# Optimization experiments

Measured on AMD Instinct MI355X. Metric: run time of the kernel, lower is better.

The kernel has to match this reference:

```python
import jax, jax.numpy as jnp
from jax import lax
import numpy as np

B, K = 32, 8
NUM_LABELS = 600
GRID = 100          # grid_size
FEATURE_DIM = 256
HUMAN = 100         # human_width == human_height


def setup_inputs() -> dict:
    rng = np.random.default_rng(0)
    ids = rng.integers(0, NUM_LABELS, size=(B, K))
    # Synthetic OA_distn: per-label MVN params (means + Cholesky factors of small covs).
    # Means chosen so sampled obj_x/obj_y are non-negative (well-defined slicing regime).
    mean_xy = rng.uniform(0.2, 0.8, size=(NUM_LABELS, 2)).astype(np.float32)
    mean_wh = rng.uniform(-0.3, 0.3, size=(NUM_LABELS, 2)).astype(np.float32)
    L = 0.05 * np.eye(2, dtype=np.float32)  # shared Cholesky factor (cov = L L^T)
    eps_xy = rng.standard_normal((B, K, 2)).astype(np.float32)
    eps_wh = rng.standard_normal((B, K, 2)).astype(np.float32)
    d_xy = mean_xy[ids] + eps_xy @ L.T      # MVN sample per (b,k): mean + L eps
    d_wh = mean_wh[ids] + eps_wh @ L.T
    delta_x, delta_y = d_xy[..., 0], d_xy[..., 1]
    delta_w, delta_h = d_wh[..., 0], d_wh[..., 1]
    # .int() truncation as in torch
    obj_x = np.clip((delta_x * HUMAN).astype(np.int32), 0, None)
    obj_y = np.clip((delta_y * HUMAN).astype(np.int32), 0, None)
    obj_w = (HUMAN * np.exp(delta_w)).astype(np.int32)
    obj_h = (HUMAN * np.exp(delta_h)).astype(np.int32)
    # global canvas size: host-side max, mirrors .max().item()
    g_w = int(np.maximum(HUMAN, obj_x + obj_w).max())
    g_h = int(np.maximum(HUMAN, obj_y + obj_h).max())
    # learned params
    ks = jax.random.split(jax.random.key(0), 3)
    conv1_w = jax.random.normal(ks[0], (16, 2, 3, 3), jnp.float32) * 0.1
    conv1_b = jnp.zeros((16,), jnp.float32)
    conv2_w = jax.random.normal(ks[1], (32, 16, 3, 3), jnp.float32) * 0.05
    conv2_b = jnp.zeros((32,), jnp.float32)
    proj_w = jax.random.normal(ks[2], (FEATURE_DIM, 32 * GRID * GRID), jnp.float32) * 0.002
    proj_b = jnp.zeros((FEATURE_DIM,), jnp.float32)
    return {
        'obj_x': jnp.asarray(obj_x), 'obj_y': jnp.asarray(obj_y),
        'obj_w': jnp.asarray(obj_w), 'obj_h': jnp.asarray(obj_h),
        'g_h': g_h, 'g_w': g_w,
        'conv1_w': conv1_w, 'conv1_b': conv1_b,
        'conv2_w': conv2_w, 'conv2_b': conv2_b,
        'proj_w': proj_w, 'proj_b': proj_b,
    }


def _binary_maps(obj_x, obj_y, obj_w, obj_h, g_h, g_w):
    # Vectorized rectangle rasterization on the (g_h, g_w) global canvas.
    b, k = obj_x.shape
    yy = jnp.arange(g_h)[None, None, :, None]   # (1,1,gH,1)
    xx = jnp.arange(g_w)[None, None, None, :]   # (1,1,1,gW)
    human = jnp.broadcast_to(((yy < HUMAN) & (xx < HUMAN)), (b, k, g_h, g_w)).astype(jnp.float32)
    ox = obj_x[..., None, None]; oy = obj_y[..., None, None]
    ow = obj_w[..., None, None]; oh = obj_h[..., None, None]
    obj = ((yy >= oy) & (yy < oy + oh) & (xx >= ox) & (xx < ox + ow)).astype(jnp.float32)
    maps = jnp.stack((human, obj), axis=2).reshape(b * k, 2, g_h, g_w)
    # bilinear, half-pixel centers, no antialias == torch F.interpolate(align_corners=False)
    return jax.image.resize(maps, (b * k, 2, GRID, GRID), method='bilinear', antialias=False)


def reference(obj_x, obj_y, obj_w, obj_h, g_h, g_w, conv1_w, conv1_b, conv2_w, conv2_b, proj_w, proj_b):
    b, k = obj_x.shape
    maps = _binary_maps(obj_x, obj_y, obj_w, obj_h, g_h, g_w)  # (B*K,2,GRID,GRID)
    dn = ('NCHW', 'OIHW', 'NCHW')
    x = lax.conv_general_dilated(maps, conv1_w, (1, 1), 'SAME', dimension_numbers=dn) + conv1_b[None, :, None, None]
    x = lax.conv_general_dilated(x, conv2_w, (1, 1), 'SAME', dimension_numbers=dn) + conv2_b[None, :, None, None]
    x = x.reshape(b * k, -1)                     # (B*K, 32*GRID*GRID), CHW order
    out = x @ proj_w.T + proj_b                  # (B*K, FEATURE_DIM)
    return out.reshape(b, k, FEATURE_DIM)
```

## Files before the change

kernel.cpp:

```cpp
#include <hip/hip_runtime.h>
#include <cstddef>

#define NS 256
#define NF 256
#define NC1 16
#define NC2 32

__global__ __launch_bounds__(256) void k_prep(
    const int* __restrict__ obx, const int* __restrict__ oby,
    const int* __restrict__ obw, const int* __restrict__ obh,
    const int* __restrict__ ghp, const int* __restrict__ gwp,
    const float* __restrict__ w1, const float* __restrict__ w2,
    const float* __restrict__ pb,
    float* __restrict__ pyT, float* __restrict__ pxT,
    float* __restrict__ hy, float* __restrict__ hx,
    float* __restrict__ Weff, float* __restrict__ base) {
  int tid = threadIdx.x;
  if (blockIdx.x == 0) {
    int n = tid;
    float gh = (float)ghp[0], gw = (float)gwp[0];
    float sy = gh / 100.0f, sx = gw / 100.0f;
    int x0 = obx[n], y0 = oby[n], w = obw[n], h = obh[n];
    for (int j = 0; j < 100; ++j) {
      float u = (j + 0.5f) * sx - 0.5f;
      int a0 = (int)floorf(u);
      float t = u - (float)a0;
      float v0 = (a0 >= x0 && a0 < x0 + w) ? 1.f : 0.f;
      float v1 = (a0 + 1 >= x0 && a0 + 1 < x0 + w) ? 1.f : 0.f;
      pxT[j * 256 + n] = (1.f - t) * v0 + t * v1;
      u = (j + 0.5f) * sy - 0.5f;
      a0 = (int)floorf(u);
      t = u - (float)a0;
      v0 = (a0 >= y0 && a0 < y0 + h) ? 1.f : 0.f;
      v1 = (a0 + 1 >= y0 && a0 + 1 < y0 + h) ? 1.f : 0.f;
      pyT[j * 256 + n] = (1.f - t) * v0 + t * v1;
    }
    if (n < 100) {
      int j = n;
      float u = (j + 0.5f) * sx - 0.5f;
      int a0 = (int)floorf(u);
      float t = u - (float)a0;
      float v0 = (a0 >= 0 && a0 < 100) ? 1.f : 0.f;
      float v1 = (a0 + 1 >= 0 && a0 + 1 < 100) ? 1.f : 0.f;
      hx[j] = (1.f - t) * v0 + t * v1;
      u = (j + 0.5f) * sy - 0.5f;
      a0 = (int)floorf(u);
      t = u - (float)a0;
      v0 = (a0 >= 0 && a0 < 100) ? 1.f : 0.f;
      v1 = (a0 + 1 >= 0 && a0 + 1 < 100) ? 1.f : 0.f;
      hy[j] = (1.f - t) * v0 + t * v1;
    }
  } else if (blockIdx.x == 1) {
    for (int idx = tid; idx < NC2 * 25; idx += 256) {
      int c2 = idx / 25, d = idx % 25;
      int dy = d / 5, dx = d % 5;
      float s = 0.f;
      for (int c1 = 0; c1 < NC1; ++c1)
        for (int sy = 0; sy < 3; ++sy) {
          int ty = dy - sy;
          if (ty < 0 || ty > 2) continue;
          for (int sx = 0; sx < 3; ++sx) {
            int tx = dx - sx;
            if (tx < 0 || tx > 2) continue;
            s += w1[((c1 * 2 + 1) * 3 + (2 - sy)) * 3 + (2 - sx)] *
                 w2[((c2 * NC1 + c1) * 9 + (2 - ty) * 3 + (2 - tx))];
          }
        }
      Weff[idx] = s;
    }
  } else {
    base[tid] = pb[tid];
  }
}

__global__ __launch_bounds__(256) void k_t1h(
    const float* __restrict__ w1, const float* __restrict__ b1,
    const float* __restrict__ hy, const float* __restrict__ hx,
    float* __restrict__ t1h) {
  int idx = blockIdx.x * 256 + threadIdx.x;
  if (idx >= NC1 * 10000) return;
  int c1 = idx / 10000, p = idx % 10000;
  int i = p / 100, j = p % 100;
  float acc = b1[c1];
  for (int dy = 0; dy < 3; ++dy) {
    int yy = i + dy - 1;
    if (yy < 0 || yy >= 100) continue;
    for (int dx = 0; dx < 3; ++dx) {
      int xx = j + dx - 1;
      if (xx < 0 || xx >= 100) continue;
      acc += w1[((c1 * 2 + 0) * 3 + dy) * 3 + dx] * hy[yy] * hx[xx];
    }
  }
  t1h[idx] = acc;
}

__global__ __launch_bounds__(256) void k_t2h(
    const float* __restrict__ w2, const float* __restrict__ b2,
    const float* __restrict__ t1h, float* __restrict__ t2h) {
  int idx = blockIdx.x * 256 + threadIdx.x;
  if (idx >= NC2 * 10000) return;
  int c2 = idx / 10000, p = idx % 10000;
  int i = p / 100, j = p % 100;
  float acc = b2[c2];
  for (int c1 = 0; c1 < NC1; ++c1)
    for (int dy = 0; dy < 3; ++dy) {
      int yy = i + dy - 1;
      if (yy < 0 || yy >= 100) continue;
      for (int dx = 0; dx < 3; ++dx) {
        int xx = j + dx - 1;
        if (xx < 0 || xx >= 100) continue;
        acc += w2[((c2 * NC1 + c1) * 9 + dy * 3 + dx)] *
               t1h[c1 * 10000 + yy * 100 + xx];
      }
    }
  t2h[idx] = acc;
}

__global__ __launch_bounds__(256) void k_adj5(
    const float* __restrict__ P, const float* __restrict__ Weff,
    const float* __restrict__ t2h, float* __restrict__ G,
    float* __restrict__ base, float* __restrict__ rimbuf) {
  __shared__ __align__(16) float buf[2][24 * 116];
  int tid = threadIdx.x;
  int f = blockIdx.y;
  int r0 = blockIdx.x * 20;
  const float* Pf = P + (size_t)f * (NC2 * 10000);
  float* rimf = rimbuf + (size_t)f * (NC2 * 400);

  auto stage = [&](float* b, int c2) {
    const float* Pc = Pf + c2 * 10000;
    float* rimc = rimf + c2 * 400;
    for (int w = tid; w < 600; w += 256) {
      int row = w / 25, k = w % 25;
      int gr = r0 - 2 + row;
      if (gr >= 0 && gr < 100) {
        float4 val = *(const float4*)(Pc + gr * 100 + k * 4);
        *(float4*)(b + row * 116 + 4 + k * 4) = val;
        if (gr == 0) *(float4*)(rimc + k * 4) = val;
        if (gr == 99) *(float4*)(rimc + 100 + k * 4) = val;
        if (k == 0) rimc[200 + gr] = val.x;
        if (k == 24) rimc[300 + gr] = val.w;
      }
    }
  };

  for (int i = tid; i < 2 * 24 * 116; i += 256) ((float*)buf)[i] = 0.f;
  __syncthreads();
  stage(buf[0], 0);

  int rowg = tid / 25, colg = tid % 25;
  bool act = rowg < 10;
  float acc[2][4] = {};
  float bacc = 0.f;

  for (int c2 = 0; c2 < NC2; ++c2) {
    __syncthreads();
    if (c2 + 1 < NC2) stage(buf[(c2 + 1) & 1], c2 + 1);
    if (act) {
      const float* lp = &buf[c2 & 1][rowg * 232 + colg * 4];
      const float* We = Weff + c2 * 25;
#pragma unroll
      for (int ir = 0; ir < 6; ++ir) {
        float4 A = *(const float4*)(lp + ir * 116);
        float4 Bv = *(const float4*)(lp + ir * 116 + 4);
        float4 Cv = *(const float4*)(lp + ir * 116 + 8);
        float v[12] = {A.x,  A.y,  A.z,  A.w,  Bv.x, Bv.y,
                       Bv.z, Bv.w, Cv.x, Cv.y, Cv.z, Cv.w};
#pragma unroll
        for (int rr = 0; rr < 2; ++rr) {
          int dy = ir - rr;
          if (dy < 0 || dy > 4) continue;
#pragma unroll
          for (int dx = 0; dx < 5; ++dx) {
            float w = We[dy * 5 + dx];
#pragma unroll
            for (int cc = 0; cc < 4; ++cc) acc[rr][cc] += w * v[2 + dx + cc];
          }
          if (dy == 2) {
            int grow = r0 + rowg * 2 + rr;
            float4 t =
                *(const float4*)(t2h + c2 * 10000 + grow * 100 + colg * 4);
            bacc += t.x * v[4] + t.y * v[5] + t.z * v[6] + t.w * v[7];
          }
        }
      }
    }
  }
  if (act) {
#pragma unroll
    for (int rr = 0; rr < 2; ++rr) {
      int grow = r0 + rowg * 2 + rr;
      *(float4*)&G[(size_t)f * 10000 + grow * 100 + colg * 4] =
          *(float4*)&acc[rr][0];
    }
  }
  __syncthreads();
  float* red = &buf[0][0];
  red[tid] = bacc;
  __syncthreads();
  for (int s = 128; s > 0; s >>= 1) {
    if (tid < s) red[tid] += red[tid + s];
    __syncthreads();
  }
  if (tid == 0) atomicAdd(&base[f], red[0]);
}

__global__ __launch_bounds__(256) void k_rim_h(
    const float* __restrict__ rimbuf, const float* __restrict__ w2,
    float* __restrict__ hpart) {
  __shared__ float rs[8 * 400];
  int tid = threadIdx.x;
  int c2g = blockIdx.x;
  int f = blockIdx.y;
  for (int i = tid; i < 3200; i += 256)
    rs[i] = rimbuf[(size_t)f * 12800 + c2g * 3200 + i];
  __syncthreads();
  for (int qq = 0; qq < 2; ++qq) {
    int j = tid + qq * 256;
    if (j >= 404) break;
    int qy, qx;
    if (j < 102) { qy = -1; qx = j - 1; }
    else if (j < 204) { qy = 100; qx = j - 103; }
    else if (j < 304) { qy = j - 204; qx = -1; }
    else { qy = j - 304; qx = 100; }
    float hacc[NC1];
#pragma unroll
    for (int c1 = 0; c1 < NC1; ++c1) hacc[c1] = 0.f;
    for (int c2l = 0; c2l < 8; ++c2l) {
      int c2 = c2g * 8 + c2l;
      for (int ty = 0; ty < 3; ++ty)
        for (int tx = 0; tx < 3; ++tx) {
          int r = qy + ty - 1, c = qx + tx - 1;
          bool ok = (r >= 0 && r < 100 && c >= 0 && c < 100);
          int side, i2;
          if (r == 0) { side = 0; i2 = c; }
          else if (r == 99) { side = 1; i2 = c; }
          else if (c == 0) { side = 2; i2 = r; }
          else { side = 3; i2 = r; }
          i2 = min(max(i2, 0), 99);
          float val = ok ? rs[c2l * 400 + side * 100 + i2] : 0.f;
#pragma unroll
          for (int c1 = 0; c1 < NC1; ++c1)
            hacc[c1] += w2[(c2 * NC1 + c1) * 9 + (2 - ty) * 3 + (2 - tx)] * val;
        }
    }
#pragma unroll
    for (int c1 = 0; c1 < NC1; ++c1)
      hpart[(((size_t)f * 4 + c2g) * NC1 + c1) * 404 + j] = hacc[c1];
  }
}

__global__ __launch_bounds__(256) void k_rim_apply(
    const float* __restrict__ hpart, const float* __restrict__ w1,
    float* __restrict__ G) {
  __shared__ float hs[NC1 * 404];
  __shared__ float w1s[288];
  int tid = threadIdx.x;
  int f = blockIdx.x;
  for (int i = tid; i < NC1 * 404; i += 256) {
    float s = 0.f;
    for (int g = 0; g < 4; ++g)
      s += hpart[((size_t)f * 4 + g) * (NC1 * 404) + i];
    hs[i] = s;
  }
  for (int i = tid; i < 288; i += 256) w1s[i] = w1[i];
  __syncthreads();
  for (int idx = tid; idx < 396; idx += 256) {
    int py, px;
    if (idx < 100) { py = 0; px = idx; }
    else if (idx < 200) { py = 99; px = idx - 100; }
    else if (idx < 298) { py = idx - 199; px = 0; }
    else { py = idx - 297; px = 99; }
    float corr = 0.f;
    for (int sy = 0; sy < 3; ++sy)
      for (int sx = 0; sx < 3; ++sx) {
        int qy = py + sy - 1, qx = px + sx - 1;
        bool ph = (qy == -1 || qy == 100 || qx == -1 || qx == 100);
        if (!ph) continue;
        int j;
        if (qy == -1) j = qx + 1;
        else if (qy == 100) j = 103 + qx;
        else if (qx == -1) j = 204 + qy;
        else j = 304 + qy;
#pragma unroll
        for (int c1 = 0; c1 < NC1; ++c1)
          corr += w1s[((c1 * 2 + 1) * 3 + (2 - sy)) * 3 + (2 - sx)] *
                  hs[c1 * 404 + j];
      }
    G[(size_t)f * 10000 + py * 100 + px] -= corr;
  }
}

__global__ __launch_bounds__(256) void k_gemm(
    const float* __restrict__ G, const float* __restrict__ pyT,
    const float* __restrict__ pxT, float* __restrict__ part) {
  __shared__ float Gs[8 * 132];
  __shared__ float Ms[8 * 128];
  int tid = threadIdx.x;
  int fT = blockIdx.x, nT = blockIdx.y, kS = blockIdx.z;
  int f0 = fT * 128, n0 = nT * 128, kb0 = kS * 80;
  int tf = tid % 16, tn = tid / 16;
  int fG = tid >> 1, kq = (tid & 1) * 4;
  int nl = tid & 127, kh = tid >> 7;
  float acc[8][8] = {};
  for (int ch = 0; ch < 10; ++ch) {
    int kb = kb0 + ch * 8;
    __syncthreads();
    {
      float4 g = *(const float4*)&G[(size_t)(f0 + fG) * 10000 + kb + kq];
      Gs[(kq + 0) * 132 + fG] = g.x;
      Gs[(kq + 1) * 132 + fG] = g.y;
      Gs[(kq + 2) * 132 + fG] = g.z;
      Gs[(kq + 3) * 132 + fG] = g.w;
    }
#pragma unroll
    for (int kk = 0; kk < 4; ++kk) {
      int k = kh * 4 + kk;
      int p = kb + k;
      int pi = p / 100, pj = p - pi * 100;
      Ms[k * 128 + nl] = pyT[pi * 256 + n0 + nl] * pxT[pj * 256 + n0 + nl];
    }
    __syncthreads();
#pragma unroll
    for (int k = 0; k < 8; ++k) {
      float4 ga = *(const float4*)&Gs[k * 132 + tf * 8];
      float4 gb = *(const float4*)&Gs[k * 132 + tf * 8 + 4];
      float4 ma = *(const float4*)&Ms[k * 128 + tn * 8];
      float4 mb = *(const float4*)&Ms[k * 128 + tn * 8 + 4];
      float gv[8] = {ga.x, ga.y, ga.z, ga.w, gb.x, gb.y, gb.z, gb.w};
      float mv[8] = {ma.x, ma.y, ma.z, ma.w, mb.x, mb.y, mb.z, mb.w};
#pragma unroll
      for (int nn = 0; nn < 8; ++nn)
#pragma unroll
        for (int ff = 0; ff < 8; ++ff) acc[nn][ff] += mv[nn] * gv[ff];
    }
  }
  size_t pb = (((size_t)kS * 2 + nT) * 2 + fT) * 16384;
#pragma unroll
  for (int nn = 0; nn < 8; ++nn) {
    int row = tn * 8 + nn;
    *(float4*)&part[pb + row * 128 + tf * 8] =
        make_float4(acc[nn][0], acc[nn][1], acc[nn][2], acc[nn][3]);
    *(float4*)&part[pb + row * 128 + tf * 8 + 4] =
        make_float4(acc[nn][4], acc[nn][5], acc[nn][6], acc[nn][7]);
  }
}

__global__ __launch_bounds__(256) void k_out(
    const float* __restrict__ part, const float* __restrict__ base,
    float* __restrict__ out) {
  int gid = blockIdx.x * 256 + threadIdx.x;
  int f = gid & 255, n = gid >> 8;
  int nT = n >> 7, nl = n & 127, fT = f >> 7, fl = f & 127;
  float val = base[f];
  size_t off = ((size_t)(nT * 2 + fT)) * 16384 + nl * 128 + fl;
  for (int s = 0; s < 125; ++s) val += part[(size_t)s * 65536 + off];
  out[(size_t)n * 256 + f] = val;
}

extern "C" void kernel_launch(void* const* d_in, const int* in_sizes, int n_in,
                              void* d_out, int out_size, void* d_ws,
                              size_t ws_size, hipStream_t stream) {
  const int* obj_x = (const int*)d_in[0];
  const int* obj_y = (const int*)d_in[1];
  const int* obj_w = (const int*)d_in[2];
  const int* obj_h = (const int*)d_in[3];
  const int* g_h = (const int*)d_in[4];
  const int* g_w = (const int*)d_in[5];
  const float* conv1_w = (const float*)d_in[6];
  const float* conv1_b = (const float*)d_in[7];
  const float* conv2_w = (const float*)d_in[8];
  const float* conv2_b = (const float*)d_in[9];
  const float* proj_w = (const float*)d_in[10];
  const float* proj_b = (const float*)d_in[11];
  float* out = (float*)d_out;

  float* w = (float*)d_ws;
  float* pyT = w;    w += 100 * 256;
  float* pxT = w;    w += 100 * 256;
  float* hy = w;     w += 100;
  float* hx = w;     w += 100;
  float* t1h = w;    w += NC1 * 10000;
  float* t2h = w;    w += NC2 * 10000;
  float* base = w;   w += NF;
  float* Weff = w;   w += NC2 * 25;
  float* G = w;      w += (size_t)NF * 10000;
  float* rimbuf = w; w += (size_t)NF * NC2 * 400;
  float* hpart = w;  w += (size_t)NF * 4 * NC1 * 404;
  float* part = w;   w += (size_t)500 * 16384;

  k_prep<<<3, 256, 0, stream>>>(obj_x, obj_y, obj_w, obj_h, g_h, g_w, conv1_w,
                                conv2_w, proj_b, pyT, pxT, hy, hx, Weff, base);
  k_t1h<<<625, 256, 0, stream>>>(conv1_w, conv1_b, hy, hx, t1h);
  k_t2h<<<1250, 256, 0, stream>>>(conv2_w, conv2_b, t1h, t2h);
  k_adj5<<<dim3(5, 256), 256, 0, stream>>>(proj_w, Weff, t2h, G, base, rimbuf);
  k_rim_h<<<dim3(4, 256), 256, 0, stream>>>(rimbuf, conv2_w, hpart);
  k_rim_apply<<<256, 256, 0, stream>>>(hpart, conv1_w, G);
  k_gemm<<<dim3(2, 2, 125), 256, 0, stream>>>(G, pyT, pxT, part);
  k_out<<<256, 256, 0, stream>>>(part, base, out);
}
```

Measured before the change: 725.3 us.

## Enlarge adj5 row tiles, fuse rim kernels, and reorder GEMM LDS reads

k_adj5 now has each block cover 40 rows and each thread 4 rows instead of 2, so fewer halo rows are loaded per output. A bounds guard handles the last partial tile, and the grid drops from 5 to 3 row blocks. The two rim kernels are merged into one per-feature kernel that keeps all 32 channels in shared memory, removing the hpart round trip through global memory and one launch. The GEMM's G-tile reads and output writes now use a split 4+4 column layout, which should cut LDS bank conflicts. The cost is fewer blocks in adj5 and the fused rim kernel, and more LDS per block (rs is 12800 floats).

```diff
diff --git a/kernel.cpp b/kernel.cpp
--- a/kernel.cpp
+++ b/kernel.cpp
@@ -120,17 +120,17 @@
     const float* __restrict__ P, const float* __restrict__ Weff,
     const float* __restrict__ t2h, float* __restrict__ G,
     float* __restrict__ base, float* __restrict__ rimbuf) {
-  __shared__ __align__(16) float buf[2][24 * 116];
+  __shared__ __align__(16) float buf[2][44 * 116];
   int tid = threadIdx.x;
   int f = blockIdx.y;
-  int r0 = blockIdx.x * 20;
+  int r0 = blockIdx.x * 40;
   const float* Pf = P + (size_t)f * (NC2 * 10000);
   float* rimf = rimbuf + (size_t)f * (NC2 * 400);
 
   auto stage = [&](float* b, int c2) {
     const float* Pc = Pf + c2 * 10000;
     float* rimc = rimf + c2 * 400;
-    for (int w = tid; w < 600; w += 256) {
+    for (int w = tid; w < 1100; w += 256) {
       int row = w / 25, k = w % 25;
       int gr = r0 - 2 + row;
       if (gr >= 0 && gr < 100) {
@@ -144,30 +144,30 @@
     }
   };
 
-  for (int i = tid; i < 2 * 24 * 116; i += 256) ((float*)buf)[i] = 0.f;
+  for (int i = tid; i < 2 * 44 * 116; i += 256) ((float*)buf)[i] = 0.f;
   __syncthreads();
   stage(buf[0], 0);
 
   int rowg = tid / 25, colg = tid % 25;
-  bool act = rowg < 10;
-  float acc[2][4] = {};
+  bool act = tid < 250;
+  float acc[4][4] = {};
   float bacc = 0.f;
 
   for (int c2 = 0; c2 < NC2; ++c2) {
     __syncthreads();
     if (c2 + 1 < NC2) stage(buf[(c2 + 1) & 1], c2 + 1);
     if (act) {
-      const float* lp = &buf[c2 & 1][rowg * 232 + colg * 4];
+      const float* lp = &buf[c2 & 1][rowg * 464 + colg * 4];
       const float* We = Weff + c2 * 25;
 #pragma unroll
-      for (int ir = 0; ir < 6; ++ir) {
+      for (int ir = 0; ir < 8; ++ir) {
         float4 A = *(const float4*)(lp + ir * 116);
         float4 Bv = *(const float4*)(lp + ir * 116 + 4);
         float4 Cv = *(const float4*)(lp + ir * 116 + 8);
         float v[12] = {A.x,  A.y,  A.z,  A.w,  Bv.x, Bv.y,
                        Bv.z, Bv.w, Cv.x, Cv.y, Cv.z, Cv.w};
 #pragma unroll
-        for (int rr = 0; rr < 2; ++rr) {
+        for (int rr = 0; rr < 4; ++rr) {
           int dy = ir - rr;
           if (dy < 0 || dy > 4) continue;
 #pragma unroll
@@ -177,10 +177,12 @@
             for (int cc = 0; cc < 4; ++cc) acc[rr][cc] += w * v[2 + dx + cc];
           }
           if (dy == 2) {
-            int grow = r0 + rowg * 2 + rr;
-            float4 t =
-                *(const float4*)(t2h + c2 * 10000 + grow * 100 + colg * 4);
-            bacc += t.x * v[4] + t.y * v[5] + t.z * v[6] + t.w * v[7];
+            int grow = r0 + rowg * 4 + rr;
+            if (grow < 100) {
+              float4 t =
+                  *(const float4*)(t2h + c2 * 10000 + grow * 100 + colg * 4);
+              bacc += t.x * v[4] + t.y * v[5] + t.z * v[6] + t.w * v[7];
+            }
           }
         }
       }
@@ -188,10 +190,11 @@
   }
   if (act) {
 #pragma unroll
-    for (int rr = 0; rr < 2; ++rr) {
-      int grow = r0 + rowg * 2 + rr;
-      *(float4*)&G[(size_t)f * 10000 + grow * 100 + colg * 4] =
-          *(float4*)&acc[rr][0];
+    for (int rr = 0; rr < 4; ++rr) {
+      int grow = r0 + rowg * 4 + rr;
+      if (grow < 100)
+        *(float4*)&G[(size_t)f * 10000 + grow * 100 + colg * 4] =
+            *(float4*)&acc[rr][0];
     }
   }
   __syncthreads();
@@ -205,15 +208,17 @@
   if (tid == 0) atomicAdd(&base[f], red[0]);
 }
 
-__global__ __launch_bounds__(256) void k_rim_h(
+__global__ __launch_bounds__(256) void k_rim(
     const float* __restrict__ rimbuf, const float* __restrict__ w2,
-    float* __restrict__ hpart) {
-  __shared__ float rs[8 * 400];
+    const float* __restrict__ w1, float* __restrict__ G) {
+  __shared__ float rs[NC2 * 400];
+  __shared__ float hs[NC1 * 404];
+  __shared__ float w1s[288];
   int tid = threadIdx.x;
-  int c2g = blockIdx.x;
-  int f = blockIdx.y;
-  for (int i = tid; i < 3200; i += 256)
-    rs[i] = rimbuf[(size_t)f * 12800 + c2g * 3200 + i];
+  int f = blockIdx.x;
+  for (int i = tid; i < NC2 * 400; i += 256)
+    rs[i] = rimbuf[(size_t)f * (NC2 * 400) + i];
+  for (int i = tid; i < 288; i += 256) w1s[i] = w1[i];
   __syncthreads();
   for (int qq = 0; qq < 2; ++qq) {
     int j = tid + qq * 256;
@@ -226,44 +231,32 @@
     float hacc[NC1];
 #pragma unroll
     for (int c1 = 0; c1 < NC1; ++c1) hacc[c1] = 0.f;
-    for (int c2l = 0; c2l < 8; ++c2l) {
-      int c2 = c2g * 8 + c2l;
-      for (int ty = 0; ty < 3; ++ty)
-        for (int tx = 0; tx < 3; ++tx) {
-          int r = qy + ty - 1, c = qx + tx - 1;
-          bool ok = (r >= 0 && r < 100 && c >= 0 && c < 100);
-          int side, i2;
-          if (r == 0) { side = 0; i2 = c; }
-          else if (r == 99) { side = 1; i2 = c; }
-          else if (c == 0) { side = 2; i2 = r; }
-          else { side = 3; i2 = r; }
-          i2 = min(max(i2, 0), 99);
-          float val = ok ? rs[c2l * 400 + side * 100 + i2] : 0.f;
-#pragma unroll
-          for (int c1 = 0; c1 < NC1; ++c1)
-            hacc[c1] += w2[(c2 * NC1 + c1) * 9 + (2 - ty) * 3 + (2 - tx)] * val;
+#pragma unroll
+    for (int ty = 0; ty < 3; ++ty)
+#pragma unroll
+      for (int tx = 0; tx < 3; ++tx) {
+        int r = qy + ty - 1, c = qx + tx - 1;
+        bool ok = (r >= 0 && r < 100 && c >= 0 && c < 100);
+        int side, i2;
+        if (r == 0) { side = 0; i2 = c; }
+        else if (r == 99) { side = 1; i2 = c; }
+        else if (c == 0) { side = 2; i2 = r; }
+        else { side = 3; i2 = r; }
+        i2 = min(max(i2, 0), 99);
+        int rbase = side * 100 + i2;
+        if (ok) {
+          for (int c2 = 0; c2 < NC2; ++c2) {
+            float val = rs[c2 * 400 + rbase];
+#pragma unroll
+            for (int c1 = 0; c1 < NC1; ++c1)
+              hacc[c1] +=
+                  w2[(c2 * NC1 + c1) * 9 + (2 - ty) * 3 + (2 - tx)] * val;
+          }
         }
-    }
-#pragma unroll
-    for (int c1 = 0; c1 < NC1; ++c1)
-      hpart[(((size_t)f * 4 + c2g) * NC1 + c1) * 404 + j] = hacc[c1];
-  }
-}
-
-__global__ __launch_bounds__(256) void k_rim_apply(
-    const float* __restrict__ hpart, const float* __restrict__ w1,
-    float* __restrict__ G) {
-  __shared__ float hs[NC1 * 404];
-  __shared__ float w1s[288];
-  int tid = threadIdx.x;
-  int f = blockIdx.x;
-  for (int i = tid; i < NC1 * 404; i += 256) {
-    float s = 0.f;
-    for (int g = 0; g < 4; ++g)
-      s += hpart[((size_t)f * 4 + g) * (NC1 * 404) + i];
-    hs[i] = s;
-  }
-  for (int i = tid; i < 288; i += 256) w1s[i] = w1[i];
+      }
+#pragma unroll
+    for (int c1 = 0; c1 < NC1; ++c1) hs[c1 * 404 + j] = hacc[c1];
+  }
   __syncthreads();
   for (int idx = tid; idx < 396; idx += 256) {
     int py, px;
@@ -323,8 +316,8 @@
     __syncthreads();
 #pragma unroll
     for (int k = 0; k < 8; ++k) {
-      float4 ga = *(const float4*)&Gs[k * 132 + tf * 8];
-      float4 gb = *(const float4*)&Gs[k * 132 + tf * 8 + 4];
+      float4 ga = *(const float4*)&Gs[k * 132 + tf * 4];
+      float4 gb = *(const float4*)&Gs[k * 132 + 64 + tf * 4];
       float4 ma = *(const float4*)&Ms[k * 128 + tn * 8];
       float4 mb = *(const float4*)&Ms[k * 128 + tn * 8 + 4];
       float gv[8] = {ga.x, ga.y, ga.z, ga.w, gb.x, gb.y, gb.z, gb.w};
@@ -339,9 +332,9 @@
 #pragma unroll
   for (int nn = 0; nn < 8; ++nn) {
     int row = tn * 8 + nn;
-    *(float4*)&part[pb + row * 128 + tf * 8] =
+    *(float4*)&part[pb + row * 128 + tf * 4] =
         make_float4(acc[nn][0], acc[nn][1], acc[nn][2], acc[nn][3]);
-    *(float4*)&part[pb + row * 128 + tf * 8 + 4] =
+    *(float4*)&part[pb + row * 128 + 64 + tf * 4] =
         make_float4(acc[nn][4], acc[nn][5], acc[nn][6], acc[nn][7]);
   }
 }
@@ -386,16 +379,14 @@
   float* Weff = w;   w += NC2 * 25;
   float* G = w;      w += (size_t)NF * 10000;
   float* rimbuf = w; w += (size_t)NF * NC2 * 400;
-  float* hpart = w;  w += (size_t)NF * 4 * NC1 * 404;
   float* part = w;   w += (size_t)500 * 16384;
 
   k_prep<<<3, 256, 0, stream>>>(obj_x, obj_y, obj_w, obj_h, g_h, g_w, conv1_w,
                                 conv2_w, proj_b, pyT, pxT, hy, hx, Weff, base);
   k_t1h<<<625, 256, 0, stream>>>(conv1_w, conv1_b, hy, hx, t1h);
   k_t2h<<<1250, 256, 0, stream>>>(conv2_w, conv2_b, t1h, t2h);
-  k_adj5<<<dim3(5, 256), 256, 0, stream>>>(proj_w, Weff, t2h, G, base, rimbuf);
-  k_rim_h<<<dim3(4, 256), 256, 0, stream>>>(rimbuf, conv2_w, hpart);
-  k_rim_apply<<<256, 256, 0, stream>>>(hpart, conv1_w, G);
+  k_adj5<<<dim3(3, 256), 256, 0, stream>>>(proj_w, Weff, t2h, G, base, rimbuf);
+  k_rim<<<256, 256, 0, stream>>>(rimbuf, conv2_w, conv1_w, G);
   k_gemm<<<dim3(2, 2, 125), 256, 0, stream>>>(G, pyT, pxT, part);
   k_out<<<256, 256, 0, stream>>>(part, base, out);
 }
```

After: 755.6 us. 4.2% more time.
